# Kernel optimization log

Hardware: AMD Instinct MI355X
Metric: run time of the kernel (lower is better)

## Reference

```python
import jax, jax.numpy as jnp
import numpy as np

B, T, C = 4, 2048, 1024


def setup_inputs() -> dict:
    key = jax.random.key(0)
    ks = jax.random.split(key, 7)
    s = 1.0 / np.sqrt(C)
    return {
        "x": jax.random.normal(ks[0], (B, T, C), dtype=jnp.float32),
        "Wq": jax.random.normal(ks[1], (C, C), dtype=jnp.float32) * s,
        "bq": jnp.zeros((C,), dtype=jnp.float32),
        "Wk": jax.random.normal(ks[2], (C, C), dtype=jnp.float32) * s,
        "bk": jnp.zeros((C,), dtype=jnp.float32),
        "Wv": jax.random.normal(ks[3], (C, C), dtype=jnp.float32) * s,
        "bv": jnp.zeros((C,), dtype=jnp.float32),
    }


def reference(x, Wq, bq, Wk, bk, Wv, bv):
    # q/k/v projections (torch Linear: x @ W^T + b; here W stored as [C_in, C_out])
    q = x @ Wq + bq  # (B, T, C)
    k = x @ Wk + bk
    v = x @ Wv + bv
    scale = 1.0 / jnp.sqrt(jnp.asarray(C, dtype=x.dtype))
    att = jnp.einsum("btc,bsc->bts", q, k) * scale  # (B, T, T)
    # causal mask: additive -inf above the diagonal
    causal = jnp.tril(jnp.ones((T, T), dtype=bool))
    att = jnp.where(causal, att, jnp.asarray(-jnp.inf, dtype=att.dtype))
    att = jax.nn.softmax(att, axis=-1)
    # dropout is identity in eval/reference mode
    out = jnp.einsum("bts,bsc->btc", att, v)  # (B, T, C)
    return out
```

## Files before the change

### kernel.cpp

```cpp
#include <hip/hip_runtime.h>

#define B_ 4
#define T_ 2048
#define C_ 1024

typedef unsigned short u16;
typedef unsigned int u32;
typedef short sh8 __attribute__((ext_vector_type(8)));
typedef float f32x4 __attribute__((ext_vector_type(4)));

__device__ float rowsum_g[4 * 2048];

__device__ __forceinline__ float bf2f(u16 u) {
    union { float f; u32 i; } c; c.i = ((u32)u) << 16; return c.f;
}
__device__ __forceinline__ u16 f2bf(float f) {
    union { float f; u32 i; } c; c.f = f;
    return (u16)((c.i + 0x7FFFu + ((c.i >> 16) & 1u)) >> 16);
}

__device__ __forceinline__ void gload_lds16(const void* g, void* l) {
    __builtin_amdgcn_global_load_lds(
        (const __attribute__((address_space(1))) u32*)g,
        (__attribute__((address_space(3))) u32*)l, 16, 0, 0);
}

__device__ __forceinline__ void wait_vm8()   { asm volatile("s_waitcnt vmcnt(8)" ::: "memory"); }
__device__ __forceinline__ void wait_vm0()   { asm volatile("s_waitcnt vmcnt(0)" ::: "memory"); }
__device__ __forceinline__ void barrier_raw(){ asm volatile("s_barrier" ::: "memory"); }

template<bool RS>
__device__ __forceinline__ void mm_core(
    const u16* __restrict__ A, const u16* __restrict__ B,
    int ldA, int ldB, int nk64,
    u16* lds, f32x4 (&acc)[4][4], f32x4* rsacc, int tid)
{
    const int w  = tid >> 6, l = tid & 63;
    const int fr = l & 15,  fq = l >> 4;
    const int wm = (w & 1) << 6, wn = (w >> 1) << 6;
    const int rl = l >> 3;
    const int pc = l & 7;
    const int cg = pc ^ rl;

    sh8 ones;
    if (RS) {
#pragma unroll
        for (int e = 0; e < 8; ++e) ones[e] = (short)0x3F80;
    }

    auto issue = [&](int kt) {
        const int ko = kt << 6;
        u16* dA = lds + ((kt & 1) << 14);
        u16* dB = dA + 8192;
#pragma unroll
        for (int t = 0; t < 4; ++t) {
            const int r0 = w * 32 + t * 8;
            const int r  = r0 + rl;
            gload_lds16(A + (size_t)r * ldA + ko + cg * 8, dA + ((size_t)r0 * 8 + l) * 8);
            gload_lds16(B + (size_t)r * ldB + ko + cg * 8, dB + ((size_t)r0 * 8 + l) * 8);
        }
    };

    issue(0);
    issue(1);

    for (int kt = 0; kt < nk64; ++kt) {
        if (kt + 1 < nk64) wait_vm8(); else wait_vm0();
        barrier_raw();
        u16* bufA = lds + ((kt & 1) << 14);
        u16* bufB = bufA + 8192;
#pragma unroll
        for (int kk = 0; kk < 2; ++kk) {
            sh8 af[4], bf[4];
            const int g = kk * 4 + fq;
#pragma unroll
            for (int i = 0; i < 4; ++i) {
                const int m = wm + i * 16 + fr;
                af[i] = *(const sh8*)(bufA + ((size_t)m * 8 + (g ^ (m & 7))) * 8);
                const int n = wn + i * 16 + fr;
                bf[i] = *(const sh8*)(bufB + ((size_t)n * 8 + (g ^ (n & 7))) * 8);
            }
#pragma unroll
            for (int i = 0; i < 4; ++i) {
#pragma unroll
                for (int j = 0; j < 4; ++j)
                    acc[i][j] = __builtin_amdgcn_mfma_f32_16x16x32_bf16(af[i], bf[j], acc[i][j], 0, 0, 0);
                if (RS)
                    rsacc[i] = __builtin_amdgcn_mfma_f32_16x16x32_bf16(af[i], ones, rsacc[i], 0, 0, 0);
            }
        }
        barrier_raw();
        if (kt + 2 < nk64) issue(kt + 2);
    }
}

__global__ __launch_bounds__(256) void cvt_all(
    const float* __restrict__ x,
    const float* __restrict__ Wq, const float* __restrict__ Wk, const float* __restrict__ Wv,
    u16* __restrict__ xb, u16* __restrict__ wt)
{
    __shared__ float tile[64][68];
    const int bid = blockIdx.x;
    if (bid >= 8960) {
        float* p = rowsum_g + (size_t)(bid - 8960) * 4096 + threadIdx.x * 16;
        const float4 z4 = {0.f, 0.f, 0.f, 0.f};
#pragma unroll
        for (int e = 0; e < 4; ++e) ((float4*)p)[e] = z4;
        return;
    }
    if (bid < 8192) {
        size_t i = ((size_t)bid * 256 + threadIdx.x) * 4;
        float4 f = *(const float4*)(x + i);
        ushort4 o;
        o.x = f2bf(f.x); o.y = f2bf(f.y); o.z = f2bf(f.z); o.w = f2bf(f.w);
        *(ushort4*)(xb + i) = o;
        return;
    }
    const int r = bid - 8192;
    const int z = r >> 8;
    const int rr = r & 255;
    const int n0 = (rr & 15) * 64, k0 = (rr >> 4) * 64;
    const float* W = z == 0 ? Wq : (z == 1 ? Wk : Wv);
    u16* out = wt + (size_t)z * C_ * C_;
    const int tx = threadIdx.x & 15, ty = threadIdx.x >> 4;
#pragma unroll
    for (int rr2 = 0; rr2 < 4; ++rr2) {
        int row = ty + rr2 * 16;
        *(float4*)&tile[row][tx * 4] = *(const float4*)(W + (size_t)(k0 + row) * C_ + n0 + tx * 4);
    }
    __syncthreads();
#pragma unroll
    for (int rr2 = 0; rr2 < 4; ++rr2) {
        int n = ty + rr2 * 16;
        ushort4 o;
        o.x = f2bf(tile[tx * 4 + 0][n]);
        o.y = f2bf(tile[tx * 4 + 1][n]);
        o.z = f2bf(tile[tx * 4 + 2][n]);
        o.w = f2bf(tile[tx * 4 + 3][n]);
        *(ushort4*)(out + (size_t)(n0 + n) * C_ + k0 + tx * 4) = o;
    }
}

__global__ __launch_bounds__(256, 2) void qkv_z(
    const u16* __restrict__ xb, const u16* __restrict__ W,
    const float* __restrict__ bias,
    u16* __restrict__ out, int isv)
{
    __shared__ __align__(16) u16 smem[32768];
    const int x = blockIdx.x;
    const int mt = ((x & 7) << 3) + (x >> 6);
    const int nt = (x >> 3) & 7;
    const int m0 = mt << 7, n0 = nt << 7;
    const int tid = threadIdx.x;
    f32x4 acc[4][4];
#pragma unroll
    for (int i = 0; i < 4; ++i)
#pragma unroll
        for (int j = 0; j < 4; ++j) acc[i][j] = 0.0f;

    mm_core<false>(xb + (size_t)m0 * C_, W + (size_t)n0 * C_, C_, C_, C_ / 64, smem, acc, nullptr, tid);

    const int w = tid >> 6, l = tid & 63, fr = l & 15, fq = l >> 4;
    const int wm = (w & 1) << 6, wn = (w >> 1) << 6;
    if (!isv) {
#pragma unroll
        for (int i = 0; i < 4; ++i)
#pragma unroll
            for (int j = 0; j < 4; ++j) {
                const int ln = wn + j * 16 + fr;
                const float bb = bias[n0 + ln];
#pragma unroll
                for (int r = 0; r < 4; ++r) {
                    const int lm = wm + i * 16 + fq * 4 + r;
                    smem[lm * 136 + ln] = f2bf(acc[i][j][r] + bb);
                }
            }
        __syncthreads();
        const int rr = tid >> 4, cc = tid & 15;
#pragma unroll
        for (int p = 0; p < 8; ++p) {
            const int row = p * 16 + rr;
            uint4 val = *(const uint4*)&smem[row * 136 + cc * 8];
            *(uint4*)(out + (size_t)(m0 + row) * C_ + n0 + cc * 8) = val;
        }
    } else {
#pragma unroll
        for (int i = 0; i < 4; ++i)
#pragma unroll
            for (int j = 0; j < 4; ++j) {
                const int ln = wn + j * 16 + fr;
                const float bb = bias[n0 + ln];
#pragma unroll
                for (int r = 0; r < 4; ++r) {
                    const int lm = wm + i * 16 + fq * 4 + r;
                    smem[lm * 129 + ln] = f2bf(acc[i][j][r] + bb);
                }
            }
        __syncthreads();
        const int b = m0 >> 11;
        const int t0 = m0 & 2047;
        u16* vt = out + (size_t)b * C_ * T_;
#pragma unroll
        for (int pass = 0; pass < 8; ++pass) {
            const int ln = (tid >> 4) + pass * 16;
            const int c  = tid & 15;
            u16 tmp[8];
#pragma unroll
            for (int e = 0; e < 8; ++e) tmp[e] = smem[(c * 8 + e) * 129 + ln];
            *(uint4*)(vt + (size_t)(n0 + ln) * T_ + t0 + c * 8) = *(uint4*)tmp;
        }
    }
}

__device__ __constant__ size_t att_off[4] = {
    0, (size_t)1 << 22, (size_t)1 << 25, ((size_t)1 << 25) + ((size_t)1 << 22)
};

__global__ __launch_bounds__(256, 2) void scores_mfma(
    const u16* __restrict__ qb, const u16* __restrict__ kb, u16* __restrict__ wsbase)
{
    const int id = blockIdx.x;
    const int s_ = (id & 7) * 68 + (id >> 3);
    const int b  = s_ / 136;
    int t = s_ - b * 136;
    int by = (int)((sqrtf(8.f * t + 1.f) - 1.f) * 0.5f);
    while ((by + 1) * (by + 2) / 2 <= t) ++by;
    while (by * (by + 1) / 2 > t) --by;
    const int bx = t - by * (by + 1) / 2;
    const int s0 = bx * 128, m0 = by * 128;
    __shared__ __align__(16) u16 smem[32768];
    const u16* Q = qb + (size_t)b * T_ * C_ + (size_t)m0 * C_;
    const u16* K = kb + (size_t)b * T_ * C_ + (size_t)s0 * C_;
    const int tid = threadIdx.x;
    f32x4 acc[4][4];
#pragma unroll
    for (int i = 0; i < 4; ++i)
#pragma unroll
        for (int j = 0; j < 4; ++j) acc[i][j] = 0.0f;

    mm_core<false>(Q, K, C_, C_, C_ / 64, smem, acc, nullptr, tid);

    const int w = tid >> 6, l = tid & 63, fr = l & 15, fq = l >> 4;
    const int wm = (w & 1) << 6, wn = (w >> 1) << 6;
#pragma unroll
    for (int i = 0; i < 4; ++i)
#pragma unroll
        for (int r = 0; r < 4; ++r) {
            const int lm = wm + i * 16 + fq * 4 + r;
            const int m = m0 + lm;
#pragma unroll
            for (int j = 0; j < 4; ++j) {
                const int ls = wn + j * 16 + fr;
                const int s = s0 + ls;
                float e = (s <= m) ? __expf(acc[i][j][r] * 0.03125f) : 0.f;
                smem[lm * 136 + ls] = f2bf(e);
            }
        }
    __syncthreads();
    u16* att = wsbase + att_off[b] + (size_t)m0 * T_ + s0;
    const int rr = tid >> 4, cc = tid & 15;
#pragma unroll
    for (int p = 0; p < 8; ++p) {
        const int row = p * 16 + rr;
        uint4 val = *(const uint4*)&smem[row * 136 + cc * 8];
        *(uint4*)(att + (size_t)row * T_ + cc * 8) = val;
    }
    {
        const int r2 = tid >> 1, half = tid & 1;
        const u16* rowp = &smem[r2 * 136 + half * 64];
        float ssum = 0.f;
#pragma unroll
        for (int e = 0; e < 64; ++e) ssum += bf2f(rowp[e]);
        ssum += __shfl_xor(ssum, 1);
        if (!half) atomicAdd(&rowsum_g[b * 2048 + m0 + r2], ssum);
    }
}

__global__ __launch_bounds__(256, 2) void pv_mfma(
    const u16* __restrict__ wsbase, const u16* __restrict__ vt,
    float* __restrict__ outp)
{
    const int b = blockIdx.z;
    const int n0 = blockIdx.x * 128;
    const int by = (blockIdx.z < 2) ? (15 - blockIdx.y) : blockIdx.y;
    const int m0 = by * 128;
    __shared__ __align__(16) u16 smem[32768];
    const u16* A  = wsbase + att_off[b] + (size_t)m0 * T_;
    const u16* Bp = vt + (size_t)b * C_ * T_ + (size_t)n0 * T_;
    const int tid = threadIdx.x;
    f32x4 acc[4][4];
#pragma unroll
    for (int i = 0; i < 4; ++i)
#pragma unroll
        for (int j = 0; j < 4; ++j) acc[i][j] = 0.0f;

    mm_core<false>(A, Bp, T_, T_, (m0 + 128) >> 6, smem, acc, nullptr, tid);

    const int w = tid >> 6, l = tid & 63, fr = l & 15, fq = l >> 4;
    const int wm = (w & 1) << 6, wn = (w >> 1) << 6;
    float* fb = (float*)smem;
#pragma unroll
    for (int p = 0; p < 2; ++p) {
        if ((w & 1) == p) {
#pragma unroll
            for (int i = 0; i < 4; ++i)
#pragma unroll
                for (int r = 0; r < 4; ++r) {
                    const int rr2 = i * 16 + fq * 4 + r;
                    const float inv = 1.0f / rowsum_g[b * 2048 + m0 + wm + rr2];
#pragma unroll
                    for (int j = 0; j < 4; ++j)
                        fb[rr2 * 132 + wn + j * 16 + fr] = acc[i][j][r] * inv;
                }
        }
        __syncthreads();
        const int rr = tid >> 5, cc = (tid & 31) * 4;
#pragma unroll
        for (int k2 = 0; k2 < 8; ++k2) {
            const int row = k2 * 8 + rr;
            float4 val = *(const float4*)&fb[row * 132 + cc];
            *(float4*)(outp + ((size_t)b * T_ + m0 + p * 64 + row) * C_ + n0 + cc) = val;
        }
        __syncthreads();
    }
}

extern "C" void kernel_launch(void* const* d_in, const int* in_sizes, int n_in,
                              void* d_out, int out_size, void* d_ws, size_t ws_size,
                              hipStream_t stream) {
    const float* x  = (const float*)d_in[0];
    const float* Wq = (const float*)d_in[1];
    const float* bq = (const float*)d_in[2];
    const float* Wk = (const float*)d_in[3];
    const float* bk = (const float*)d_in[4];
    const float* Wv = (const float*)d_in[5];
    const float* bv = (const float*)d_in[6];
    float* out = (float*)d_out;

    char* ws = (char*)d_ws;
    u16* xb   = (u16*)ws;
    u16* q    = (u16*)(ws + (16ull << 20));
    u16* k    = (u16*)(ws + (32ull << 20));
    u16* vt   = (u16*)(ws + (48ull << 20));
    u16* wt   = (u16*)(ws + (64ull << 20));
    u16* attb = (u16*)ws;

    cvt_all <<<8962, 256, 0, stream>>>(x, Wq, Wk, Wv, xb, wt);
    qkv_z   <<<512, 256, 0, stream>>>(xb, wt,                   bq, q,  0);
    qkv_z   <<<512, 256, 0, stream>>>(xb, wt + (size_t)C_*C_,   bk, k,  0);
    qkv_z   <<<512, 256, 0, stream>>>(xb, wt + (size_t)2*C_*C_, bv, vt, 1);
    scores_mfma<<<544, 256, 0, stream>>>(q, k, attb);
    pv_mfma    <<<dim3(8, 16, 4), 256, 0, stream>>>(attb, vt, out);
}
```

Baseline: 224.6 us.

## Merge QKV launches and fuse scores and PV via per-row completion counters

```diff
diff --git a/kernel.cpp b/kernel.cpp
--- a/kernel.cpp
+++ b/kernel.cpp
@@ -10,6 +10,7 @@
 typedef float f32x4 __attribute__((ext_vector_type(4)));
 
 __device__ float rowsum_g[4 * 2048];
+__device__ int   row_done_g[64];
 
 __device__ __forceinline__ float bf2f(u16 u) {
     union { float f; u32 i; } c; c.i = ((u32)u) << 16; return c.f;
@@ -106,6 +107,7 @@
         const float4 z4 = {0.f, 0.f, 0.f, 0.f};
 #pragma unroll
         for (int e = 0; e < 4; ++e) ((float4*)p)[e] = z4;
+        if (bid == 8960 && threadIdx.x < 64) row_done_g[threadIdx.x] = 0;
         return;
     }
     if (bid < 8192) {
@@ -141,16 +143,20 @@
     }
 }
 
-__global__ __launch_bounds__(256, 2) void qkv_z(
-    const u16* __restrict__ xb, const u16* __restrict__ W,
-    const float* __restrict__ bias,
-    u16* __restrict__ out, int isv)
+__global__ __launch_bounds__(256, 2) void qkv_f(
+    const u16* __restrict__ xb, const u16* __restrict__ wt,
+    const float* __restrict__ bq, const float* __restrict__ bk, const float* __restrict__ bv,
+    u16* __restrict__ qo, u16* __restrict__ ko, u16* __restrict__ vto)
 {
     __shared__ __align__(16) u16 smem[32768];
     const int x = blockIdx.x;
-    const int mt = ((x & 7) << 3) + (x >> 6);
-    const int nt = (x >> 3) & 7;
+    const int z = x >> 9;
+    const int inner = x & 511;
+    const int mt = ((inner & 7) << 3) + (inner >> 6);
+    const int nt = (inner >> 3) & 7;
     const int m0 = mt << 7, n0 = nt << 7;
+    const u16* W = wt + (size_t)z * C_ * C_;
+    const float* bias = z == 0 ? bq : (z == 1 ? bk : bv);
     const int tid = threadIdx.x;
     f32x4 acc[4][4];
 #pragma unroll
@@ -162,7 +168,7 @@
 
     const int w = tid >> 6, l = tid & 63, fr = l & 15, fq = l >> 4;
     const int wm = (w & 1) << 6, wn = (w >> 1) << 6;
-    if (!isv) {
+    if (z < 2) {
 #pragma unroll
         for (int i = 0; i < 4; ++i)
 #pragma unroll
@@ -176,6 +182,7 @@
                 }
             }
         __syncthreads();
+        u16* out = z == 0 ? qo : ko;
         const int rr = tid >> 4, cc = tid & 15;
 #pragma unroll
         for (int p = 0; p < 8; ++p) {
@@ -199,7 +206,7 @@
         __syncthreads();
         const int b = m0 >> 11;
         const int t0 = m0 & 2047;
-        u16* vt = out + (size_t)b * C_ * T_;
+        u16* vt = vto + (size_t)b * C_ * T_;
 #pragma unroll
         for (int pass = 0; pass < 8; ++pass) {
             const int ln = (tid >> 4) + pass * 16;
@@ -216,112 +223,123 @@
     0, (size_t)1 << 22, (size_t)1 << 25, ((size_t)1 << 25) + ((size_t)1 << 22)
 };
 
-__global__ __launch_bounds__(256, 2) void scores_mfma(
-    const u16* __restrict__ qb, const u16* __restrict__ kb, u16* __restrict__ wsbase)
-{
-    const int id = blockIdx.x;
-    const int s_ = (id & 7) * 68 + (id >> 3);
-    const int b  = s_ / 136;
-    int t = s_ - b * 136;
-    int by = (int)((sqrtf(8.f * t + 1.f) - 1.f) * 0.5f);
-    while ((by + 1) * (by + 2) / 2 <= t) ++by;
-    while (by * (by + 1) / 2 > t) --by;
-    const int bx = t - by * (by + 1) / 2;
-    const int s0 = bx * 128, m0 = by * 128;
-    __shared__ __align__(16) u16 smem[32768];
-    const u16* Q = qb + (size_t)b * T_ * C_ + (size_t)m0 * C_;
-    const u16* K = kb + (size_t)b * T_ * C_ + (size_t)s0 * C_;
-    const int tid = threadIdx.x;
-    f32x4 acc[4][4];
-#pragma unroll
-    for (int i = 0; i < 4; ++i)
-#pragma unroll
-        for (int j = 0; j < 4; ++j) acc[i][j] = 0.0f;
-
-    mm_core<false>(Q, K, C_, C_, C_ / 64, smem, acc, nullptr, tid);
-
-    const int w = tid >> 6, l = tid & 63, fr = l & 15, fq = l >> 4;
-    const int wm = (w & 1) << 6, wn = (w >> 1) << 6;
-#pragma unroll
-    for (int i = 0; i < 4; ++i)
-#pragma unroll
-        for (int r = 0; r < 4; ++r) {
-            const int lm = wm + i * 16 + fq * 4 + r;
-            const int m = m0 + lm;
-#pragma unroll
-            for (int j = 0; j < 4; ++j) {
-                const int ls = wn + j * 16 + fr;
-                const int s = s0 + ls;
-                float e = (s <= m) ? __expf(acc[i][j][r] * 0.03125f) : 0.f;
-                smem[lm * 136 + ls] = f2bf(e);
-            }
-        }
-    __syncthreads();
-    u16* att = wsbase + att_off[b] + (size_t)m0 * T_ + s0;
-    const int rr = tid >> 4, cc = tid & 15;
-#pragma unroll
-    for (int p = 0; p < 8; ++p) {
-        const int row = p * 16 + rr;
-        uint4 val = *(const uint4*)&smem[row * 136 + cc * 8];
-        *(uint4*)(att + (size_t)row * T_ + cc * 8) = val;
-    }
-    {
-        const int r2 = tid >> 1, half = tid & 1;
-        const u16* rowp = &smem[r2 * 136 + half * 64];
-        float ssum = 0.f;
-#pragma unroll
-        for (int e = 0; e < 64; ++e) ssum += bf2f(rowp[e]);
-        ssum += __shfl_xor(ssum, 1);
-        if (!half) atomicAdd(&rowsum_g[b * 2048 + m0 + r2], ssum);
-    }
-}
-
-__global__ __launch_bounds__(256, 2) void pv_mfma(
-    const u16* __restrict__ wsbase, const u16* __restrict__ vt,
+__global__ __launch_bounds__(256, 2) void att_fused(
+    const u16* __restrict__ qb, const u16* __restrict__ kb,
+    const u16* __restrict__ vt, u16* __restrict__ wsbase,
     float* __restrict__ outp)
 {
-    const int b = blockIdx.z;
-    const int n0 = blockIdx.x * 128;
-    const int by = (blockIdx.z < 2) ? (15 - blockIdx.y) : blockIdx.y;
-    const int m0 = by * 128;
     __shared__ __align__(16) u16 smem[32768];
-    const u16* A  = wsbase + att_off[b] + (size_t)m0 * T_;
-    const u16* Bp = vt + (size_t)b * C_ * T_ + (size_t)n0 * T_;
+    const int id = blockIdx.x;
     const int tid = threadIdx.x;
-    f32x4 acc[4][4];
-#pragma unroll
-    for (int i = 0; i < 4; ++i)
-#pragma unroll
-        for (int j = 0; j < 4; ++j) acc[i][j] = 0.0f;
-
-    mm_core<false>(A, Bp, T_, T_, (m0 + 128) >> 6, smem, acc, nullptr, tid);
-
-    const int w = tid >> 6, l = tid & 63, fr = l & 15, fq = l >> 4;
-    const int wm = (w & 1) << 6, wn = (w >> 1) << 6;
-    float* fb = (float*)smem;
-#pragma unroll
-    for (int p = 0; p < 2; ++p) {
-        if ((w & 1) == p) {
-#pragma unroll
-            for (int i = 0; i < 4; ++i)
-#pragma unroll
-                for (int r = 0; r < 4; ++r) {
-                    const int rr2 = i * 16 + fq * 4 + r;
-                    const float inv = 1.0f / rowsum_g[b * 2048 + m0 + wm + rr2];
-#pragma unroll
-                    for (int j = 0; j < 4; ++j)
-                        fb[rr2 * 132 + wn + j * 16 + fr] = acc[i][j][r] * inv;
+
+    if (id < 544) {
+        int r = 15, off = 0;
+        while (id >= off + 4 * (r + 1)) { off += 4 * (r + 1); --r; }
+        const int rem = id - off;
+        const int b = rem & 3, bx = rem >> 2, by = r;
+        const int s0 = bx * 128, m0 = by * 128;
+        const u16* Q = qb + (size_t)b * T_ * C_ + (size_t)m0 * C_;
+        const u16* K = kb + (size_t)b * T_ * C_ + (size_t)s0 * C_;
+        f32x4 acc[4][4];
+#pragma unroll
+        for (int i = 0; i < 4; ++i)
+#pragma unroll
+            for (int j = 0; j < 4; ++j) acc[i][j] = 0.0f;
+
+        mm_core<false>(Q, K, C_, C_, C_ / 64, smem, acc, nullptr, tid);
+
+        const int w = tid >> 6, l = tid & 63, fr = l & 15, fq = l >> 4;
+        const int wm = (w & 1) << 6, wn = (w >> 1) << 6;
+#pragma unroll
+        for (int i = 0; i < 4; ++i)
+#pragma unroll
+            for (int rr = 0; rr < 4; ++rr) {
+                const int lm = wm + i * 16 + fq * 4 + rr;
+                const int m = m0 + lm;
+#pragma unroll
+                for (int j = 0; j < 4; ++j) {
+                    const int ls = wn + j * 16 + fr;
+                    const int s = s0 + ls;
+                    float e = (s <= m) ? __expf(acc[i][j][rr] * 0.03125f) : 0.f;
+                    smem[lm * 136 + ls] = f2bf(e);
                 }
-        }
-        __syncthreads();
-        const int rr = tid >> 5, cc = (tid & 31) * 4;
-#pragma unroll
-        for (int k2 = 0; k2 < 8; ++k2) {
-            const int row = k2 * 8 + rr;
-            float4 val = *(const float4*)&fb[row * 132 + cc];
-            *(float4*)(outp + ((size_t)b * T_ + m0 + p * 64 + row) * C_ + n0 + cc) = val;
-        }
-        __syncthreads();
+            }
+        __syncthreads();
+        u16* att = wsbase + att_off[b] + (size_t)m0 * T_ + s0;
+        {
+            const int rr = tid >> 4, cc = tid & 15;
+#pragma unroll
+            for (int p = 0; p < 8; ++p) {
+                const int row = p * 16 + rr;
+                uint4 val = *(const uint4*)&smem[row * 136 + cc * 8];
+                *(uint4*)(att + (size_t)row * T_ + cc * 8) = val;
+            }
+        }
+        {
+            const int r2 = tid >> 1, half = tid & 1;
+            const u16* rowp = &smem[r2 * 136 + half * 64];
+            float ssum = 0.f;
+#pragma unroll
+            for (int e = 0; e < 64; ++e) ssum += bf2f(rowp[e]);
+            ssum += __shfl_xor(ssum, 1);
+            if (!half) atomicAdd(&rowsum_g[b * 2048 + m0 + r2], ssum);
+        }
+        __syncthreads();
+        if (tid == 0) {
+            __threadfence();
+            atomicAdd(&row_done_g[b * 16 + by], 1);
+        }
+    } else {
+        const int pid = id - 544;
+        const int m = 15 - (pid >> 5);
+        const int rem = pid & 31;
+        const int b = rem & 3, n = rem >> 2;
+        const int n0 = n << 7, m0 = m << 7;
+
+        if (tid == 0) {
+            while (atomicAdd(&row_done_g[b * 16 + m], 0) < m + 1)
+                __builtin_amdgcn_s_sleep(32);
+            __threadfence();
+        }
+        __syncthreads();
+
+        const u16* A  = wsbase + att_off[b] + (size_t)m0 * T_;
+        const u16* Bp = vt + (size_t)b * C_ * T_ + (size_t)n0 * T_;
+        f32x4 acc[4][4];
+#pragma unroll
+        for (int i = 0; i < 4; ++i)
+#pragma unroll
+            for (int j = 0; j < 4; ++j) acc[i][j] = 0.0f;
+
+        mm_core<false>(A, Bp, T_, T_, (m0 + 128) >> 6, smem, acc, nullptr, tid);
+
+        const int w = tid >> 6, l = tid & 63, fr = l & 15, fq = l >> 4;
+        const int wm = (w & 1) << 6, wn = (w >> 1) << 6;
+        float* fb = (float*)smem;
+#pragma unroll
+        for (int p = 0; p < 2; ++p) {
+            if ((w & 1) == p) {
+#pragma unroll
+                for (int i = 0; i < 4; ++i)
+#pragma unroll
+                    for (int rr = 0; rr < 4; ++rr) {
+                        const int rr2 = i * 16 + fq * 4 + rr;
+                        const float inv = 1.0f / rowsum_g[b * 2048 + m0 + wm + rr2];
+#pragma unroll
+                        for (int j = 0; j < 4; ++j)
+                            fb[rr2 * 132 + wn + j * 16 + fr] = acc[i][j][rr] * inv;
+                    }
+            }
+            __syncthreads();
+            const int rr = tid >> 5, cc = (tid & 31) * 4;
+#pragma unroll
+            for (int k2 = 0; k2 < 8; ++k2) {
+                const int row = k2 * 8 + rr;
+                float4 val = *(const float4*)&fb[row * 132 + cc];
+                *(float4*)(outp + ((size_t)b * T_ + m0 + p * 64 + row) * C_ + n0 + cc) = val;
+            }
+            __syncthreads();
+        }
     }
 }
 
@@ -345,10 +363,7 @@
     u16* wt   = (u16*)(ws + (64ull << 20));
     u16* attb = (u16*)ws;
 
-    cvt_all <<<8962, 256, 0, stream>>>(x, Wq, Wk, Wv, xb, wt);
-    qkv_z   <<<512, 256, 0, stream>>>(xb, wt,                   bq, q,  0);
-    qkv_z   <<<512, 256, 0, stream>>>(xb, wt + (size_t)C_*C_,   bk, k,  0);
-    qkv_z   <<<512, 256, 0, stream>>>(xb, wt + (size_t)2*C_*C_, bv, vt, 1);
-    scores_mfma<<<544, 256, 0, stream>>>(q, k, attb);
-    pv_mfma    <<<dim3(8, 16, 4), 256, 0, stream>>>(attb, vt, out);
-}
+    cvt_all  <<<8962, 256, 0, stream>>>(x, Wq, Wk, Wv, xb, wt);
+    qkv_f    <<<1536, 256, 0, stream>>>(xb, wt, bq, bk, bv, q, k, vt);
+    att_fused<<<1056, 256, 0, stream>>>(q, k, vt, attb, out);
+}
```

After: 237.7 us. +5.8%, slower.
